# Kernel optimization log

Measured on AMD Instinct MI355X. Metric: run time of the kernel, lower is better.

## Reference

```python
import jax, jax.numpy as jnp
import numpy as np

NUM_COMPONENTS = 4
HEADS = 16

def setup_inputs() -> dict:
    key = jax.random.key(0)
    ks = jax.random.split(key, 7)
    BC, S, D = 8, 4096, 1024   # batch*components, latent tokens, hidden dim
    E = 160                     # encoder (text) sequence length
    w_scale = 0.02              # keep logits in a sane range
    return {
        "hidden_states": jax.random.normal(ks[0], (BC, S, D), jnp.float32),
        "encoder_hidden_states": jax.random.normal(ks[1], (BC, E, D), jnp.float32),
        "Wq": jax.random.normal(ks[2], (D, D), jnp.float32) * w_scale,
        "Wk": jax.random.normal(ks[3], (D, D), jnp.float32) * w_scale,
        "Wv": jax.random.normal(ks[4], (D, D), jnp.float32) * w_scale,
        "Wo": jax.random.normal(ks[5], (D, D), jnp.float32) * w_scale,
        "bo": jnp.zeros((D,), jnp.float32),
    }

def reference(hidden_states, encoder_hidden_states, Wq, Wk, Wv, Wo, bo):
    BC, S, D = hidden_states.shape
    E = encoder_hidden_states.shape[1]
    C = NUM_COMPONENTS
    B = BC // C
    H = HEADS
    dh = D // H
    scale = dh ** -0.5

    # projections (diffusers to_q/to_k/to_v, no bias)
    q = hidden_states @ Wq            # [BC, S, D]
    k = encoder_hidden_states @ Wk    # [BC, E, D]
    v = encoder_hidden_states @ Wv    # [BC, E, D]

    q = q.reshape(BC, S, H, dh).transpose(0, 2, 1, 3)  # [BC, H, S, dh]
    k = k.reshape(BC, E, H, dh).transpose(0, 2, 1, 3)  # [BC, H, E, dh]
    v = v.reshape(BC, E, H, dh).transpose(0, 2, 1, 3)  # [BC, H, E, dh]

    scores = jnp.einsum("bhsd,bhtd->bhst", q, k) * scale  # [BC, H, S, E]
    scores_c = scores.reshape(C, B, H, S, E)

    # pooled (mean over encoder tokens) softmax across components
    pooled = scores_c.mean(axis=-1, keepdims=True)         # [C, B, H, S, 1]
    weights_pooled = jax.nn.softmax(pooled, axis=0)        # softmax over components
    # per-row softmax over encoder tokens, scaled by component weight
    weights = jax.nn.softmax(scores_c, axis=-1) * weights_pooled
    weights = weights.reshape(BC, H, S, E)

    out = jnp.einsum("bhst,bhtd->bhsd", weights, v)        # [BC, H, S, dh]
    out = out.transpose(0, 2, 1, 3).reshape(BC, S, D)

    out = out @ Wo + bo        # to_out[0]; to_out[1] is dropout (identity, eval)
    out = out + hidden_states  # residual_connection=True, rescale factor 1
    return out
```

## Files before the change

### kernel.cpp

```cpp
#include <hip/hip_runtime.h>
#include <stdint.h>

typedef __attribute__((ext_vector_type(8))) short short8;
typedef __attribute__((ext_vector_type(4))) float f32x4;
typedef __attribute__((ext_vector_type(4))) unsigned short us4;

#define DI __device__ __forceinline__

static constexpr int Dm = 1024;
static constexpr int Sm = 4096;
static constexpr int Em = 160;
static constexpr int Hm = 16;

static constexpr size_t OFF_HSB  = 0;
static constexpr size_t OFF_WT   = 67108864;
static constexpr size_t OFF_QB   = 75497472;
static constexpr size_t OFF_KB   = 142606336;
static constexpr size_t OFF_VT   = 147849216;
static constexpr size_t OFF_EHSB = 150994944;

DI unsigned short f2b(float f) {
  union { float f; unsigned u; } x; x.f = f;
  unsigned r = x.u + 0x7fffu + ((x.u >> 16) & 1u);
  return (unsigned short)(r >> 16);
}

DI void gl_lds16(const void* g, void* l) {
  __builtin_amdgcn_global_load_lds(
      (const __attribute__((address_space(1))) unsigned int*)g,
      (__attribute__((address_space(3))) unsigned int*)l, 16, 0, 0);
}

__global__ void k_prep0(const float* __restrict__ ehs, unsigned short* __restrict__ eb,
                        const float* __restrict__ W0, const float* __restrict__ W1,
                        const float* __restrict__ W2, const float* __restrict__ W3,
                        unsigned short* __restrict__ Wt) {
  __shared__ float t[32][33];
  const int bid = blockIdx.x, tid = threadIdx.x;
  if (bid < 4096) {
    const int bz = bid >> 10, rest = bid & 1023, by = rest >> 5, bx = rest & 31;
    const float* W = (bz == 0) ? W0 : (bz == 1) ? W1 : (bz == 2) ? W2 : W3;
    unsigned short* o = Wt + (size_t)bz * 1048576;
    const int tx = tid & 31, ty = tid >> 5;
    const int n = bx * 32 + tx, k0 = by * 32;
    #pragma unroll
    for (int j = ty; j < 32; j += 8) t[j][tx] = W[(size_t)(k0 + j) * 1024 + n];
    __syncthreads();
    #pragma unroll
    for (int j = ty; j < 32; j += 8)
      o[(size_t)(bx * 32 + j) * 1024 + k0 + tx] = f2b(t[tx][j]);
  } else {
    const int i = (bid - 4096) * 256 + tid;
    float4 v = ((const float4*)ehs)[i];
    us4 o = { f2b(v.x), f2b(v.y), f2b(v.z), f2b(v.w) };
    *(us4*)(eb + (size_t)i * 4) = o;
  }
}

__global__ __launch_bounds__(256, 2) void k_prep1(const float* __restrict__ hs,
                                                  unsigned short* __restrict__ hsb,
                                                  const unsigned short* __restrict__ eb,
                                                  const unsigned short* __restrict__ Wt,
                                                  unsigned short* __restrict__ kb,
                                                  unsigned short* __restrict__ vt) {
  __shared__ __align__(16) char smem[32768];
  const int bid = blockIdx.x, tid = threadIdx.x;
  if (bid >= 160) {
    const int stride = 2048 * 256;
    for (int i = (bid - 160) * 256 + tid; i < 8388608; i += stride) {
      float4 v = ((const float4*)hs)[i];
      us4 o = { f2b(v.x), f2b(v.y), f2b(v.z), f2b(v.w) };
      *(us4*)(hsb + (size_t)i * 4) = o;
    }
    return;
  }
  char* As = smem;
  char* Bs = smem + 16384;
  const int lane = tid & 63;
  const int l15 = lane & 15;
  const int g = lane >> 4;
  const int wv = tid >> 6;
  const int wr = wv >> 1, wc = wv & 1;
  const int z = bid / 80, rr = bid - z * 80;
  const int m0 = (rr % 10) * 128, n0 = (rr / 10) * 128;
  const unsigned short* Bt = Wt + (size_t)(1 + z) * 1048576;

  f32x4 acc[4][4];
  #pragma unroll
  for (int i = 0; i < 4; ++i)
    #pragma unroll
    for (int j = 0; j < 4; ++j) acc[i][j] = (f32x4){0.f, 0.f, 0.f, 0.f};

  for (int t = 0; t < 16; ++t) {
    __syncthreads();
    #pragma unroll
    for (int is = 0; is < 4; ++is) {
      int ch = is * 256 + tid;
      int row = ch >> 3, j = ch & 7;
      int sj = (j ^ (row & 7)) * 8;
      gl_lds16(eb + (size_t)(m0 + row) * 1024 + t * 64 + sj, As + ch * 16);
      gl_lds16(Bt + (size_t)(n0 + row) * 1024 + t * 64 + sj, Bs + ch * 16);
    }
    __syncthreads();
    short8 af[2][4], bf[2][4];
    #pragma unroll
    for (int kk = 0; kk < 2; ++kk)
      #pragma unroll
      for (int mt = 0; mt < 4; ++mt) {
        af[kk][mt] = *(const short8*)(As + (wr * 64 + mt * 16 + l15) * 128 + ((kk * 64 + g * 16) ^ ((l15 & 7) << 4)));
        bf[kk][mt] = *(const short8*)(Bs + (wc * 64 + mt * 16 + l15) * 128 + ((kk * 64 + g * 16) ^ ((l15 & 7) << 4)));
      }
    #pragma unroll
    for (int kk = 0; kk < 2; ++kk)
      #pragma unroll
      for (int mt = 0; mt < 4; ++mt)
        #pragma unroll
        for (int nt = 0; nt < 4; ++nt)
          acc[mt][nt] = __builtin_amdgcn_mfma_f32_16x16x32_bf16(af[kk][mt], bf[kk][nt], acc[mt][nt], 0, 0, 0);
  }

  #pragma unroll
  for (int mt = 0; mt < 4; ++mt)
    #pragma unroll
    for (int nt = 0; nt < 4; ++nt)
      #pragma unroll
      for (int r = 0; r < 4; ++r) {
        int row = m0 + wr * 64 + mt * 16 + 4 * g + r;
        int col = n0 + wc * 64 + nt * 16 + l15;
        unsigned short hv = f2b(acc[mt][nt][r]);
        if (z == 0) {
          kb[(size_t)row * 1024 + col] = hv;
        } else {
          int bc = row / 160, e = row - bc * 160;
          vt[((size_t)(bc * 16 + (col >> 6)) * 64 + (col & 63)) * 192 + e] = hv;
        }
      }
}

template<int MODE>
__global__ __launch_bounds__(256, 2) void k_gemm128(const unsigned short* __restrict__ A,
                                                    const unsigned short* __restrict__ Bt,
                                                    void* __restrict__ Cout,
                                                    const float* __restrict__ bias,
                                                    const float* __restrict__ resid) {
  __shared__ __align__(16) char smem[32768];
  char* As = smem;
  char* Bs = smem + 16384;
  const int tid = threadIdx.x;
  const int lane = tid & 63;
  const int l15 = lane & 15;
  const int g = lane >> 4;
  const int wv = tid >> 6;
  const int wr = wv >> 1, wc = wv & 1;
  const int bid = blockIdx.x;
  const int m0 = ((bid >> 6) * 8 + (bid & 7)) * 128;
  const int n0 = ((bid >> 3) & 7) * 128;

  f32x4 acc[4][4];
  #pragma unroll
  for (int i = 0; i < 4; ++i)
    #pragma unroll
    for (int j = 0; j < 4; ++j) acc[i][j] = (f32x4){0.f, 0.f, 0.f, 0.f};

  for (int t = 0; t < 16; ++t) {
    __syncthreads();
    #pragma unroll
    for (int is = 0; is < 4; ++is) {
      int ch = is * 256 + tid;
      int row = ch >> 3, j = ch & 7;
      int sj = (j ^ (row & 7)) * 8;
      gl_lds16(A  + (size_t)(m0 + row) * 1024 + t * 64 + sj, As + ch * 16);
      gl_lds16(Bt + (size_t)(n0 + row) * 1024 + t * 64 + sj, Bs + ch * 16);
    }
    __syncthreads();
    short8 af[2][4], bf[2][4];
    #pragma unroll
    for (int kk = 0; kk < 2; ++kk)
      #pragma unroll
      for (int mt = 0; mt < 4; ++mt) {
        af[kk][mt] = *(const short8*)(As + (wr * 64 + mt * 16 + l15) * 128 + ((kk * 64 + g * 16) ^ ((l15 & 7) << 4)));
        bf[kk][mt] = *(const short8*)(Bs + (wc * 64 + mt * 16 + l15) * 128 + ((kk * 64 + g * 16) ^ ((l15 & 7) << 4)));
      }
    #pragma unroll
    for (int kk = 0; kk < 2; ++kk)
      #pragma unroll
      for (int mt = 0; mt < 4; ++mt)
        #pragma unroll
        for (int nt = 0; nt < 4; ++nt)
          acc[mt][nt] = __builtin_amdgcn_mfma_f32_16x16x32_bf16(af[kk][mt], bf[kk][nt], acc[mt][nt], 0, 0, 0);
  }

  if (MODE == 0) {
    __syncthreads();
    unsigned short* Cl = (unsigned short*)smem;
    #pragma unroll
    for (int mt = 0; mt < 4; ++mt)
      #pragma unroll
      for (int nt = 0; nt < 4; ++nt)
        #pragma unroll
        for (int r = 0; r < 4; ++r)
          Cl[(wr * 64 + mt * 16 + 4 * g + r) * 128 + wc * 64 + nt * 16 + l15] = f2b(acc[mt][nt][r]);
    __syncthreads();
    #pragma unroll
    for (int j = 0; j < 8; ++j) {
      int ch = j * 256 + tid;
      int row = ch >> 4, sl = ch & 15;
      *(short8*)((unsigned short*)Cout + (size_t)(m0 + row) * 1024 + n0 + sl * 8) =
          *(const short8*)(Cl + row * 128 + sl * 8);
    }
  } else {
    #pragma unroll
    for (int mt = 0; mt < 4; ++mt)
      #pragma unroll
      for (int nt = 0; nt < 4; ++nt)
        #pragma unroll
        for (int r = 0; r < 4; ++r) {
          size_t row = (size_t)(m0 + wr * 64 + mt * 16 + 4 * g + r);
          int col = n0 + wc * 64 + nt * 16 + l15;
          size_t idx = row * 1024 + col;
          ((float*)Cout)[idx] = acc[mt][nt][r] + bias[col] + resid[idx];
        }
  }
}

__global__ __launch_bounds__(256, 2) void k_attn(const unsigned short* __restrict__ Qb,
                                                 const unsigned short* __restrict__ Kb,
                                                 const unsigned short* __restrict__ Vt,
                                                 unsigned short* __restrict__ AOb) {
  __shared__ __align__(16) char smem[22528];
  float* pooled = (float*)(smem + 21504);
  const int tid = threadIdx.x, lane = tid & 63, wv = tid >> 6;
  const int g = lane >> 4, l15 = lane & 15;
  const int s0 = blockIdx.x * 64;
  const int h = blockIdx.y;
  const int b = blockIdx.z;
  const int bc = wv * 2 + b;
  const float scale = 0.125f;

  const unsigned short* Qp = Qb + ((size_t)bc * Sm + s0) * Dm + h * 64;
  const unsigned short* Kp = Kb + (size_t)bc * Em * Dm + h * 64;
  const unsigned short* Vp = Vt + ((size_t)bc * Hm + h) * (64 * 192);
  unsigned short* Op = AOb + ((size_t)bc * Sm + s0) * Dm + h * 64;
  char* Pw = smem + wv * 5376;

  #pragma unroll 1
  for (int st = 0; st < 4; ++st) {
    short8 qf[2];
    #pragma unroll
    for (int kk = 0; kk < 2; ++kk)
      qf[kk] = *(const short8*)(Qp + (size_t)(st * 16 + l15) * Dm + kk * 32 + g * 8);
    f32x4 sc[10];
    #pragma unroll
    for (int et = 0; et < 10; ++et) {
      sc[et] = (f32x4){0.f, 0.f, 0.f, 0.f};
      #pragma unroll
      for (int kk = 0; kk < 2; ++kk) {
        short8 kf = *(const short8*)(Kp + (size_t)(et * 16 + l15) * Dm + kk * 32 + g * 8);
        sc[et] = __builtin_amdgcn_mfma_f32_16x16x32_bf16(qf[kk], kf, sc[et], 0, 0, 0);
      }
    }
    float rs4[4];
    #pragma unroll
    for (int r = 0; r < 4; ++r) {
      float v = 0.f;
      #pragma unroll
      for (int et = 0; et < 10; ++et) v += sc[et][r];
      v += __shfl_xor(v, 1); v += __shfl_xor(v, 2); v += __shfl_xor(v, 4); v += __shfl_xor(v, 8);
      if (l15 == 0) pooled[(st * 16 + 4 * g + r) * 4 + wv] = v * (scale / 160.f);
      float mx = sc[0][r];
      #pragma unroll
      for (int et = 1; et < 10; ++et) mx = fmaxf(mx, sc[et][r]);
      mx = fmaxf(mx, __shfl_xor(mx, 1)); mx = fmaxf(mx, __shfl_xor(mx, 2));
      mx = fmaxf(mx, __shfl_xor(mx, 4)); mx = fmaxf(mx, __shfl_xor(mx, 8));
      float rs = 0.f;
      #pragma unroll
      for (int et = 0; et < 10; ++et) {
        float p = __expf((sc[et][r] - mx) * scale);
        rs += p;
        *(unsigned short*)(Pw + (4 * g + r) * 336 + (et * 16 + l15) * 2) = f2b(p);
      }
      rs += __shfl_xor(rs, 1); rs += __shfl_xor(rs, 2); rs += __shfl_xor(rs, 4); rs += __shfl_xor(rs, 8);
      rs4[r] = rs;
    }
    f32x4 oa[4];
    #pragma unroll
    for (int dt = 0; dt < 4; ++dt) oa[dt] = (f32x4){0.f, 0.f, 0.f, 0.f};
    #pragma unroll
    for (int k5 = 0; k5 < 5; ++k5) {
      short8 pf = *(const short8*)(Pw + l15 * 336 + k5 * 64 + g * 16);
      #pragma unroll
      for (int dt = 0; dt < 4; ++dt) {
        short8 vf = *(const short8*)(Vp + (size_t)(dt * 16 + l15) * 192 + k5 * 32 + g * 8);
        oa[dt] = __builtin_amdgcn_mfma_f32_16x16x32_bf16(pf, vf, oa[dt], 0, 0, 0);
      }
    }
    __syncthreads();
    #pragma unroll
    for (int r = 0; r < 4; ++r) {
      float4 pl = *(const float4*)&pooled[(st * 16 + 4 * g + r) * 4];
      float m3 = fmaxf(fmaxf(pl.x, pl.y), fmaxf(pl.z, pl.w));
      float ssum = __expf(pl.x - m3) + __expf(pl.y - m3) + __expf(pl.z - m3) + __expf(pl.w - m3);
      float mine = (wv == 0) ? pl.x : (wv == 1) ? pl.y : (wv == 2) ? pl.z : pl.w;
      float srw = __expf(mine - m3) / (ssum * rs4[r]);
      #pragma unroll
      for (int dt = 0; dt < 4; ++dt)
        Op[(size_t)(st * 16 + 4 * g + r) * Dm + dt * 16 + l15] = f2b(oa[dt][r] * srw);
    }
  }
}

extern "C" void kernel_launch(void* const* d_in, const int* in_sizes, int n_in,
                              void* d_out, int out_size, void* d_ws, size_t ws_size,
                              hipStream_t stream) {
  const float* hs  = (const float*)d_in[0];
  const float* ehs = (const float*)d_in[1];
  const float* Wq  = (const float*)d_in[2];
  const float* Wk  = (const float*)d_in[3];
  const float* Wv  = (const float*)d_in[4];
  const float* Wo  = (const float*)d_in[5];
  const float* bo  = (const float*)d_in[6];
  char* ws = (char*)d_ws;
  unsigned short* hsb = (unsigned short*)(ws + OFF_HSB);
  unsigned short* wt  = (unsigned short*)(ws + OFF_WT);
  unsigned short* qb  = (unsigned short*)(ws + OFF_QB);
  unsigned short* kb  = (unsigned short*)(ws + OFF_KB);
  unsigned short* vt  = (unsigned short*)(ws + OFF_VT);
  unsigned short* eb  = (unsigned short*)(ws + OFF_EHSB);

  hipLaunchKernelGGL(k_prep0, dim3(4096 + 1280), dim3(256), 0, stream, ehs, eb, Wq, Wk, Wv, Wo, wt);
  hipLaunchKernelGGL(k_prep1, dim3(160 + 2048), dim3(256), 0, stream, hs, hsb, eb, wt, kb, vt);
  hipLaunchKernelGGL((k_gemm128<0>), dim3(2048), dim3(256), 0, stream, hsb, wt, (void*)qb,
                     (const float*)nullptr, (const float*)nullptr);
  hipLaunchKernelGGL(k_attn, dim3(64, 16, 2), dim3(256), 0, stream, qb, kb, vt, hsb);
  hipLaunchKernelGGL((k_gemm128<1>), dim3(2048), dim3(256), 0, stream, hsb, wt + 3 * 1048576, d_out, bo, hs);
}
```

Baseline: 327.9 us.

## Merge prep and QKV GEMM launches, reuse Q buffer, read bf16 residual

Folds the hidden-state bf16 conversion into the first prep kernel and runs the K/V projection GEMM and the Q projection GEMM as one launch, cutting the kernel count from five to four. Attention now writes its output in place over the Q buffer. The output GEMM reads the residual from the bf16 copy of hidden_states instead of the fp32 original, and uses nontemporal loads and stores. The aim is less launch overhead and less memory traffic, at the cost of rounding the residual term to bf16.

```diff
diff --git a/kernel.cpp b/kernel.cpp
--- a/kernel.cpp
+++ b/kernel.cpp
@@ -25,16 +25,21 @@
   return (unsigned short)(r >> 16);
 }
 
+DI float b2f(unsigned short h) {
+  union { unsigned u; float f; } x; x.u = ((unsigned)h) << 16; return x.f;
+}
+
 DI void gl_lds16(const void* g, void* l) {
   __builtin_amdgcn_global_load_lds(
       (const __attribute__((address_space(1))) unsigned int*)g,
       (__attribute__((address_space(3))) unsigned int*)l, 16, 0, 0);
 }
 
-__global__ void k_prep0(const float* __restrict__ ehs, unsigned short* __restrict__ eb,
-                        const float* __restrict__ W0, const float* __restrict__ W1,
-                        const float* __restrict__ W2, const float* __restrict__ W3,
-                        unsigned short* __restrict__ Wt) {
+__global__ void k_prep(const float* __restrict__ ehs, unsigned short* __restrict__ eb,
+                       const float* __restrict__ hs, unsigned short* __restrict__ hsb,
+                       const float* __restrict__ W0, const float* __restrict__ W1,
+                       const float* __restrict__ W2, const float* __restrict__ W3,
+                       unsigned short* __restrict__ Wt) {
   __shared__ float t[32][33];
   const int bid = blockIdx.x, tid = threadIdx.x;
   if (bid < 4096) {
@@ -49,41 +54,49 @@
     #pragma unroll
     for (int j = ty; j < 32; j += 8)
       o[(size_t)(bx * 32 + j) * 1024 + k0 + tx] = f2b(t[tx][j]);
-  } else {
+  } else if (bid < 5376) {
     const int i = (bid - 4096) * 256 + tid;
     float4 v = ((const float4*)ehs)[i];
     us4 o = { f2b(v.x), f2b(v.y), f2b(v.z), f2b(v.w) };
     *(us4*)(eb + (size_t)i * 4) = o;
-  }
-}
-
-__global__ __launch_bounds__(256, 2) void k_prep1(const float* __restrict__ hs,
-                                                  unsigned short* __restrict__ hsb,
-                                                  const unsigned short* __restrict__ eb,
-                                                  const unsigned short* __restrict__ Wt,
-                                                  unsigned short* __restrict__ kb,
-                                                  unsigned short* __restrict__ vt) {
-  __shared__ __align__(16) char smem[32768];
-  const int bid = blockIdx.x, tid = threadIdx.x;
-  if (bid >= 160) {
-    const int stride = 2048 * 256;
-    for (int i = (bid - 160) * 256 + tid; i < 8388608; i += stride) {
+  } else {
+    for (int i = (bid - 5376) * 256 + tid; i < 8388608; i += 2048 * 256) {
       float4 v = ((const float4*)hs)[i];
       us4 o = { f2b(v.x), f2b(v.y), f2b(v.z), f2b(v.w) };
       *(us4*)(hsb + (size_t)i * 4) = o;
     }
-    return;
-  }
+  }
+}
+
+__global__ __launch_bounds__(256, 2) void k_gemm_qkv(const unsigned short* __restrict__ hsb,
+                                                     const unsigned short* __restrict__ eb,
+                                                     const unsigned short* __restrict__ Wt,
+                                                     unsigned short* __restrict__ qb,
+                                                     unsigned short* __restrict__ kb,
+                                                     unsigned short* __restrict__ vt) {
+  __shared__ __align__(16) char smem[32768];
   char* As = smem;
   char* Bs = smem + 16384;
+  const int bid = blockIdx.x, tid = threadIdx.x;
   const int lane = tid & 63;
   const int l15 = lane & 15;
   const int g = lane >> 4;
   const int wv = tid >> 6;
   const int wr = wv >> 1, wc = wv & 1;
-  const int z = bid / 80, rr = bid - z * 80;
-  const int m0 = (rr % 10) * 128, n0 = (rr / 10) * 128;
-  const unsigned short* Bt = Wt + (size_t)(1 + z) * 1048576;
+
+  const bool isKV = (bid < 160);
+  int m0, n0;
+  const unsigned short *Ap, *Bt;
+  if (isKV) {
+    const int z = bid / 80, rr = bid - z * 80;
+    m0 = (rr % 10) * 128; n0 = (rr / 10) * 128;
+    Ap = eb; Bt = Wt + (size_t)(1 + z) * 1048576;
+  } else {
+    const int q = bid - 160;
+    m0 = ((q >> 6) * 8 + (q & 7)) * 128;
+    n0 = ((q >> 3) & 7) * 128;
+    Ap = hsb; Bt = Wt;
+  }
 
   f32x4 acc[4][4];
   #pragma unroll
@@ -98,7 +111,7 @@
       int ch = is * 256 + tid;
       int row = ch >> 3, j = ch & 7;
       int sj = (j ^ (row & 7)) * 8;
-      gl_lds16(eb + (size_t)(m0 + row) * 1024 + t * 64 + sj, As + ch * 16);
+      gl_lds16(Ap + (size_t)(m0 + row) * 1024 + t * 64 + sj, As + ch * 16);
       gl_lds16(Bt + (size_t)(n0 + row) * 1024 + t * 64 + sj, Bs + ch * 16);
     }
     __syncthreads();
@@ -119,30 +132,50 @@
           acc[mt][nt] = __builtin_amdgcn_mfma_f32_16x16x32_bf16(af[kk][mt], bf[kk][nt], acc[mt][nt], 0, 0, 0);
   }
 
-  #pragma unroll
-  for (int mt = 0; mt < 4; ++mt)
-    #pragma unroll
-    for (int nt = 0; nt < 4; ++nt)
-      #pragma unroll
-      for (int r = 0; r < 4; ++r) {
-        int row = m0 + wr * 64 + mt * 16 + 4 * g + r;
-        int col = n0 + wc * 64 + nt * 16 + l15;
-        unsigned short hv = f2b(acc[mt][nt][r]);
-        if (z == 0) {
-          kb[(size_t)row * 1024 + col] = hv;
-        } else {
-          int bc = row / 160, e = row - bc * 160;
-          vt[((size_t)(bc * 16 + (col >> 6)) * 64 + (col & 63)) * 192 + e] = hv;
+  if (isKV) {
+    const int z = bid / 80;
+    #pragma unroll
+    for (int mt = 0; mt < 4; ++mt)
+      #pragma unroll
+      for (int nt = 0; nt < 4; ++nt)
+        #pragma unroll
+        for (int r = 0; r < 4; ++r) {
+          int row = m0 + wr * 64 + mt * 16 + 4 * g + r;
+          int col = n0 + wc * 64 + nt * 16 + l15;
+          unsigned short hv = f2b(acc[mt][nt][r]);
+          if (z == 0) {
+            kb[(size_t)row * 1024 + col] = hv;
+          } else {
+            int bc = row / 160, e = row - bc * 160;
+            vt[((size_t)(bc * 16 + (col >> 6)) * 64 + (col & 63)) * 192 + e] = hv;
+          }
         }
-      }
-}
-
-template<int MODE>
-__global__ __launch_bounds__(256, 2) void k_gemm128(const unsigned short* __restrict__ A,
-                                                    const unsigned short* __restrict__ Bt,
-                                                    void* __restrict__ Cout,
-                                                    const float* __restrict__ bias,
-                                                    const float* __restrict__ resid) {
+  } else {
+    __syncthreads();
+    unsigned short* Cl = (unsigned short*)smem;
+    #pragma unroll
+    for (int mt = 0; mt < 4; ++mt)
+      #pragma unroll
+      for (int nt = 0; nt < 4; ++nt)
+        #pragma unroll
+        for (int r = 0; r < 4; ++r)
+          Cl[(wr * 64 + mt * 16 + 4 * g + r) * 128 + wc * 64 + nt * 16 + l15] = f2b(acc[mt][nt][r]);
+    __syncthreads();
+    #pragma unroll
+    for (int j = 0; j < 8; ++j) {
+      int ch = j * 256 + tid;
+      int row = ch >> 4, sl = ch & 15;
+      __builtin_nontemporal_store(*(const short8*)(Cl + row * 128 + sl * 8),
+          (short8*)(qb + (size_t)(m0 + row) * 1024 + n0 + sl * 8));
+    }
+  }
+}
+
+__global__ __launch_bounds__(256, 2) void k_gemm_o(const unsigned short* __restrict__ A,
+                                                   const unsigned short* __restrict__ Bt,
+                                                   float* __restrict__ Cout,
+                                                   const float* __restrict__ bias,
+                                                   const unsigned short* __restrict__ residb) {
   __shared__ __align__(16) char smem[32768];
   char* As = smem;
   char* Bs = smem + 16384;
@@ -190,43 +223,23 @@
           acc[mt][nt] = __builtin_amdgcn_mfma_f32_16x16x32_bf16(af[kk][mt], bf[kk][nt], acc[mt][nt], 0, 0, 0);
   }
 
-  if (MODE == 0) {
-    __syncthreads();
-    unsigned short* Cl = (unsigned short*)smem;
-    #pragma unroll
-    for (int mt = 0; mt < 4; ++mt)
-      #pragma unroll
-      for (int nt = 0; nt < 4; ++nt)
-        #pragma unroll
-        for (int r = 0; r < 4; ++r)
-          Cl[(wr * 64 + mt * 16 + 4 * g + r) * 128 + wc * 64 + nt * 16 + l15] = f2b(acc[mt][nt][r]);
-    __syncthreads();
-    #pragma unroll
-    for (int j = 0; j < 8; ++j) {
-      int ch = j * 256 + tid;
-      int row = ch >> 4, sl = ch & 15;
-      *(short8*)((unsigned short*)Cout + (size_t)(m0 + row) * 1024 + n0 + sl * 8) =
-          *(const short8*)(Cl + row * 128 + sl * 8);
-    }
-  } else {
-    #pragma unroll
-    for (int mt = 0; mt < 4; ++mt)
-      #pragma unroll
-      for (int nt = 0; nt < 4; ++nt)
-        #pragma unroll
-        for (int r = 0; r < 4; ++r) {
-          size_t row = (size_t)(m0 + wr * 64 + mt * 16 + 4 * g + r);
-          int col = n0 + wc * 64 + nt * 16 + l15;
-          size_t idx = row * 1024 + col;
-          ((float*)Cout)[idx] = acc[mt][nt][r] + bias[col] + resid[idx];
-        }
-  }
-}
-
-__global__ __launch_bounds__(256, 2) void k_attn(const unsigned short* __restrict__ Qb,
+  #pragma unroll
+  for (int mt = 0; mt < 4; ++mt)
+    #pragma unroll
+    for (int nt = 0; nt < 4; ++nt)
+      #pragma unroll
+      for (int r = 0; r < 4; ++r) {
+        size_t row = (size_t)(m0 + wr * 64 + mt * 16 + 4 * g + r);
+        int col = n0 + wc * 64 + nt * 16 + l15;
+        size_t idx = row * 1024 + col;
+        unsigned short rh = __builtin_nontemporal_load(residb + idx);
+        __builtin_nontemporal_store(acc[mt][nt][r] + bias[col] + b2f(rh), Cout + idx);
+      }
+}
+
+__global__ __launch_bounds__(256, 2) void k_attn(unsigned short* __restrict__ Qb,
                                                  const unsigned short* __restrict__ Kb,
-                                                 const unsigned short* __restrict__ Vt,
-                                                 unsigned short* __restrict__ AOb) {
+                                                 const unsigned short* __restrict__ Vt) {
   __shared__ __align__(16) char smem[22528];
   float* pooled = (float*)(smem + 21504);
   const int tid = threadIdx.x, lane = tid & 63, wv = tid >> 6;
@@ -237,10 +250,9 @@
   const int bc = wv * 2 + b;
   const float scale = 0.125f;
 
-  const unsigned short* Qp = Qb + ((size_t)bc * Sm + s0) * Dm + h * 64;
+  unsigned short* Qp = Qb + ((size_t)bc * Sm + s0) * Dm + h * 64;
   const unsigned short* Kp = Kb + (size_t)bc * Em * Dm + h * 64;
   const unsigned short* Vp = Vt + ((size_t)bc * Hm + h) * (64 * 192);
-  unsigned short* Op = AOb + ((size_t)bc * Sm + s0) * Dm + h * 64;
   char* Pw = smem + wv * 5376;
 
   #pragma unroll 1
@@ -304,7 +316,7 @@
       float srw = __expf(mine - m3) / (ssum * rs4[r]);
       #pragma unroll
       for (int dt = 0; dt < 4; ++dt)
-        Op[(size_t)(st * 16 + 4 * g + r) * Dm + dt * 16 + l15] = f2b(oa[dt][r] * srw);
+        Qp[(size_t)(st * 16 + 4 * g + r) * Dm + dt * 16 + l15] = f2b(oa[dt][r] * srw);
     }
   }
 }
@@ -327,10 +339,8 @@
   unsigned short* vt  = (unsigned short*)(ws + OFF_VT);
   unsigned short* eb  = (unsigned short*)(ws + OFF_EHSB);
 
-  hipLaunchKernelGGL(k_prep0, dim3(4096 + 1280), dim3(256), 0, stream, ehs, eb, Wq, Wk, Wv, Wo, wt);
-  hipLaunchKernelGGL(k_prep1, dim3(160 + 2048), dim3(256), 0, stream, hs, hsb, eb, wt, kb, vt);
-  hipLaunchKernelGGL((k_gemm128<0>), dim3(2048), dim3(256), 0, stream, hsb, wt, (void*)qb,
-                     (const float*)nullptr, (const float*)nullptr);
-  hipLaunchKernelGGL(k_attn, dim3(64, 16, 2), dim3(256), 0, stream, qb, kb, vt, hsb);
-  hipLaunchKernelGGL((k_gemm128<1>), dim3(2048), dim3(256), 0, stream, hsb, wt + 3 * 1048576, d_out, bo, hs);
-}
+  hipLaunchKernelGGL(k_prep, dim3(7424), dim3(256), 0, stream, ehs, eb, hs, hsb, Wq, Wk, Wv, Wo, wt);
+  hipLaunchKernelGGL(k_gemm_qkv, dim3(2208), dim3(256), 0, stream, hsb, eb, wt, qb, kb, vt);
+  hipLaunchKernelGGL(k_attn, dim3(64, 16, 2), dim3(256), 0, stream, qb, kb, vt);
+  hipLaunchKernelGGL(k_gemm_o, dim3(2048), dim3(256), 0, stream, qb, wt + 3 * 1048576, (float*)d_out, bo, hsb);
+}
```

Result: slower. 348.4 us (+6.2%).
